# Performance work log

Measured on AMD Instinct MI355X. Metric: run time of the kernel, lower is better.

## Reference

```python
import jax, jax.numpy as jnp
import numpy as np

D = 160          # SDF grid resolution (D1=D2=D3=D)
LEVEL = 0.0      # marching_cubes(-sdf, level=-0) == level 0 on s = -sdf
N_SMOOTH = 2
LAMBD = 1.0


def _extract_mesh_np():
    """Host-side isosurface extraction (mirrors the module's CPU round-trip).
    Uses marching tetrahedra (6-tet cube decomposition) in place of skimage's
    lewiner marching cubes; topo_correct (undefined in source) is identity.
    Returns (verts [V,3] f32 in normalized coords, faces [F,3] i32, edges [E,2] i32).
    """
    xs = np.arange(D, dtype=np.float32)
    X, Y, Z = np.meshgrid(xs, xs, xs, indexing='ij')
    ctr = (D - 1) / 2.0
    sdf = np.sqrt((X - ctr) ** 2 + (Y - ctr) ** 2 + (Z - ctr) ** 2) - 0.35 * D
    sdf = sdf + 3.0 * np.sin(0.20 * X) * np.sin(0.17 * Y) * np.sin(0.23 * Z)
    s = (-sdf).astype(np.float32)  # extract level-0 isosurface of -sdf
    sflat = s.ravel()
    Ng = D ** 3

    corner_off = [(0, 0, 0), (1, 0, 0), (1, 1, 0), (0, 1, 0),
                  (0, 0, 1), (1, 0, 1), (1, 1, 1), (0, 1, 1)]
    b = np.arange(D - 1)
    BX, BY, BZ = np.meshgrid(b, b, b, indexing='ij')
    BX, BY, BZ = BX.ravel(), BY.ravel(), BZ.ravel()
    gid8 = [((BX + dx) * D + (BY + dy)) * D + (BZ + dz) for dx, dy, dz in corner_off]
    val8 = [sflat[g] for g in gid8]

    TETS = [(0, 5, 1, 6), (0, 1, 2, 6), (0, 2, 3, 6),
            (0, 3, 7, 6), (0, 7, 4, 6), (0, 4, 5, 6)]
    TE = [(0, 1), (0, 2), (0, 3), (1, 2), (1, 3), (2, 3)]  # tet edges
    CASE_TRIS = {1: [(0, 1, 2)], 14: [(0, 1, 2)],
                 2: [(0, 3, 4)], 13: [(0, 3, 4)],
                 4: [(1, 3, 5)], 11: [(1, 3, 5)],
                 8: [(2, 4, 5)], 7: [(2, 4, 5)],
                 3: [(1, 3, 4), (1, 4, 2)], 12: [(1, 3, 4), (1, 4, 2)],
                 5: [(0, 3, 5), (0, 5, 2)], 10: [(0, 3, 5), (0, 5, 2)],
                 6: [(0, 4, 5), (0, 5, 1)], 9: [(0, 4, 5), (0, 5, 1)]}
    bitw = np.array([1, 2, 4, 8])

    tri_keys = []
    for tet in TETS:
        tv = np.stack([val8[c] for c in tet], 1)  # [Nc,4] corner values
        tg = np.stack([gid8[c] for c in tet], 1)  # [Nc,4] corner grid ids
        case = (tv < LEVEL).astype(np.int64) @ bitw
        for c, tris in CASE_TRIS.items():
            sel = np.nonzero(case == c)[0]
            if sel.size == 0:
                continue
            g = tg[sel]
            for tri in tris:
                cols = []
                for e in tri:
                    i, j = TE[e]
                    lo = np.minimum(g[:, i], g[:, j])
                    hi = np.maximum(g[:, i], g[:, j])
                    cols.append(lo * Ng + hi)  # canonical grid-edge key
                tri_keys.append(np.stack(cols, 1))
    tris = np.concatenate(tri_keys, 0)  # [F,3] edge keys
    uk, inv = np.unique(tris, return_inverse=True)
    faces = inv.reshape(-1, 3).astype(np.int32)
    ga = uk // Ng
    gb = uk % Ng
    pa = np.stack(np.unravel_index(ga, (D, D, D)), 1).astype(np.float32)
    pb = np.stack(np.unravel_index(gb, (D, D, D)), 1).astype(np.float32)
    sa = sflat[ga]
    sb = sflat[gb]
    t = ((LEVEL - sa) / (sb - sa)).astype(np.float32)
    verts = pa + t[:, None] * (pb - pa)
    verts = (2.0 * verts - np.float32(D)) / np.float32(D)  # (2v-[D1,D2,D3])/D
    e = np.concatenate([faces[:, [0, 1]], faces[:, [1, 2]], faces[:, [2, 0]]], 0)
    e = np.unique(np.sort(e, 1), axis=0).astype(np.int32)
    return verts.astype(np.float32), faces, e


def setup_inputs() -> dict:
    verts, faces, edges = _extract_mesh_np()
    return {
        'v': jnp.asarray(verts)[None],      # [1,V,3]
        'edges': jnp.asarray(edges),        # [E,2] unique undirected mesh edges
        'faces': jnp.asarray(faces)[None],  # [1,F,3]
    }


def reference(v, edges, faces):
    # Uniform laplacian smoothing: v <- v + lambd * (mean_neighbor(v) - v), x2
    V = v.shape[1]
    src = jnp.concatenate([edges[:, 0], edges[:, 1]])
    dst = jnp.concatenate([edges[:, 1], edges[:, 0]])
    x = v[0]
    deg = jax.ops.segment_sum(jnp.ones(src.shape[0], x.dtype), src, num_segments=V)
    inv_deg = 1.0 / jnp.maximum(deg, 1.0)
    for _ in range(N_SMOOTH):
        nbr = jax.ops.segment_sum(x[dst], src, num_segments=V)
        x = x + LAMBD * (nbr * inv_deg[:, None] - x)
    return x, faces[0]
```

## Files before the change

kernel.cpp:

```cpp
#include <hip/hip_runtime.h>
#include <stdint.h>

#define K_ELL 32
#define K_OVF 16
#define RNG   2048
#define RW    (RNG + RNG)
#define BB    256
#define UA    6
#define UN    6
#define UF    4
#define GBS   1024
#define HALO  4096
#define SPAN  (GBS + 2 * HALO)
#define SMEM_STG (SPAN * (int)sizeof(float4))

__global__ __launch_bounds__(BB) void build_kernel(
        const int2* __restrict__ edges, int* __restrict__ offs_a,
        int* __restrict__ cntN, int* __restrict__ cntF, int* __restrict__ deg_ovf,
        int* __restrict__ adjN, int* __restrict__ adjF, int* __restrict__ adj_ovf,
        const int* __restrict__ faces, float* __restrict__ out_f,
        const float* __restrict__ v, float4* __restrict__ v4,
        int E, int V, int F3) {
    const int t = (int)blockIdx.x * BB + (int)threadIdx.x;
    const int T = (int)gridDim.x * BB;
    for (int i = t; i < E; i += T) {
        int2 e = edges[i];
        int rel = e.y - (e.x & ~(RNG - 1)) - 1;
        if (rel < RNG) {
            int r = atomicAdd(&cntN[e.y], 1);
            if (r < K_ELL) adjN[(size_t)r * V + e.y] = e.x;
        } else if (rel < RW) {
            int r = atomicAdd(&cntF[e.y], 1);
            if (r < K_ELL) adjF[(size_t)r * V + e.y] = e.x;
        } else {
            int r = atomicAdd(&deg_ovf[e.y], 1);
            if (r < K_OVF) adj_ovf[(size_t)r * V + e.y] = e.x;
        }
    }
    for (int i = t; i <= E; i += T) {
        if (i < E) {
            int lo = (i == 0) ? 0 : edges[i - 1].x + 1;
            int hi = edges[i].x;
            for (int a = lo; a <= hi; ++a) offs_a[a] = i;
        } else {
            int lo = (E > 0) ? edges[E - 1].x + 1 : 0;
            for (int a = lo; a <= V; ++a) offs_a[a] = E;
        }
    }
    if ((((uintptr_t)out_f | (uintptr_t)faces) & 15) == 0) {
        int n4 = F3 >> 2;
        const int4* f4 = (const int4*)faces;
        float4* o4 = (float4*)out_f;
        for (int j = t; j < n4; j += T) {
            int4 a = f4[j];
            o4[j] = make_float4((float)a.x, (float)a.y, (float)a.z, (float)a.w);
        }
        for (int j = (n4 << 2) + t; j < F3; j += T) out_f[j] = (float)faces[j];
    } else {
        for (int j = t; j < F3; j += T) out_f[j] = (float)faces[j];
    }
    if (((uintptr_t)v & 15) == 0) {
        const float4* vv = (const float4*)v;
        int n4v = V >> 2;
        for (int q = t; q < n4v; q += T) {
            float4 a = vv[3 * q], b = vv[3 * q + 1], c = vv[3 * q + 2];
            v4[4 * q + 0] = make_float4(a.x, a.y, a.z, 0.f);
            v4[4 * q + 1] = make_float4(a.w, b.x, b.y, 0.f);
            v4[4 * q + 2] = make_float4(b.z, b.w, c.x, 0.f);
            v4[4 * q + 3] = make_float4(c.y, c.z, c.w, 0.f);
        }
        for (int u = (n4v << 2) + t; u < V; u += T)
            v4[u] = make_float4(v[3 * u], v[3 * u + 1], v[3 * u + 2], 0.f);
    } else {
        for (int u = t; u < V; u += T)
            v4[u] = make_float4(v[3 * u], v[3 * u + 1], v[3 * u + 2], 0.f);
    }
}

template <bool PAD>
__global__ __launch_bounds__(GBS) void gather_staged(
        const float4* __restrict__ x4, const int2* __restrict__ edges,
        const int* __restrict__ offs_a,
        const int* __restrict__ cntN, const int* __restrict__ cntF,
        const int* __restrict__ deg_ovf,
        const int* __restrict__ adjN, const int* __restrict__ adjF,
        const int* __restrict__ adj_ovf,
        float* __restrict__ y, int V, int E) {
    extern __shared__ float4 tile[];
    const int c0   = (int)blockIdx.x * GBS;
    const int base = c0 - HALO;
    const int u    = c0 + (int)threadIdx.x;
    int aBeg = 0, da = 0, cN = 0, cF = 0, dO = 0;
    int gA[UA], gN[UN], gF[UF];
    if (u < V) {
        aBeg = offs_a[u];
        int aEnd = offs_a[u + 1];
        da = aEnd - aBeg;
        cN = cntN[u]; cF = cntF[u]; dO = deg_ovf[u];
        #pragma unroll
        for (int j = 0; j < UA; ++j) gA[j] = edges[min(aBeg + j, E - 1)].y;
        #pragma unroll
        for (int k = 0; k < UN; ++k) gN[k] = adjN[(size_t)k * V + u];
        #pragma unroll
        for (int k = 0; k < UF; ++k) gF[k] = adjF[(size_t)k * V + u];
    }
    for (int s = (int)threadIdx.x; s < SPAN; s += GBS) {
        int g = base + s;
        tile[s] = (g >= 0 && g < V) ? x4[g] : make_float4(0.f, 0.f, 0.f, 0.f);
    }
    __syncthreads();
    if (u >= V) return;
    int kN = cN > K_ELL ? K_ELL : cN;
    int kF = cF > K_ELL ? K_ELL : cF;
    float s0 = 0.f, s1 = 0.f, s2 = 0.f;
    #pragma unroll
    for (int j = 0; j < UA; ++j) {
        int g = (j < da) ? gA[j] : u;
        float m = (j < da) ? 1.f : 0.f;
        unsigned r = (unsigned)(g - base);
        float4 p = (r < (unsigned)SPAN) ? tile[r] : x4[g];
        s0 += m * p.x; s1 += m * p.y; s2 += m * p.z;
    }
    for (int j = UA; j < da; ++j) {
        float4 p = x4[edges[aBeg + j].y];
        s0 += p.x; s1 += p.y; s2 += p.z;
    }
    #pragma unroll
    for (int k = 0; k < UN; ++k) {
        int g = (k < kN) ? gN[k] : u;
        float m = (k < kN) ? 1.f : 0.f;
        unsigned r = (unsigned)(g - base);
        float4 p = (r < (unsigned)SPAN) ? tile[r] : x4[g];
        s0 += m * p.x; s1 += m * p.y; s2 += m * p.z;
    }
    for (int k = UN; k < kN; ++k) {
        float4 p = x4[adjN[(size_t)k * V + u]];
        s0 += p.x; s1 += p.y; s2 += p.z;
    }
    #pragma unroll
    for (int k = 0; k < UF; ++k) {
        int g = (k < kF) ? gF[k] : u;
        float m = (k < kF) ? 1.f : 0.f;
        unsigned r = (unsigned)(g - base);
        float4 p = (r < (unsigned)SPAN) ? tile[r] : x4[g];
        s0 += m * p.x; s1 += m * p.y; s2 += m * p.z;
    }
    for (int k = UF; k < kF; ++k) {
        float4 p = x4[adjF[(size_t)k * V + u]];
        s0 += p.x; s1 += p.y; s2 += p.z;
    }
    int kO = dO > K_OVF ? K_OVF : dO;
    for (int k = 0; k < kO; ++k) {
        float4 p = x4[adj_ovf[(size_t)k * V + u]];
        s0 += p.x; s1 += p.y; s2 += p.z;
    }
    int d = da + cN + cF + dO;
    float inv = 1.0f / fmaxf((float)d, 1.0f);
    if (PAD) {
        ((float4*)y)[u] = make_float4(s0 * inv, s1 * inv, s2 * inv, 0.f);
    } else {
        y[3 * u + 0] = s0 * inv;
        y[3 * u + 1] = s1 * inv;
        y[3 * u + 2] = s2 * inv;
    }
}

extern "C" void kernel_launch(void* const* d_in, const int* in_sizes, int n_in,
                              void* d_out, int out_size, void* d_ws, size_t ws_size,
                              hipStream_t stream) {
    const float* v     = (const float*)d_in[0];
    const int2*  edges = (const int2*)d_in[1];
    const int*   faces = (const int*)d_in[2];

    const int V3 = in_sizes[0];
    const int V  = V3 / 3;
    const int E  = in_sizes[1] / 2;
    const int F3 = in_sizes[2];

    float* out_v = (float*)d_out;
    float* out_f = (float*)d_out + V3;

    float4* v4      = (float4*)d_ws;
    float4* x1      = v4 + V;
    int*    adjN    = (int*)(x1 + V);
    int*    adjF    = adjN + (size_t)K_ELL * V;
    int*    adj_ovf = adjF + (size_t)K_ELL * V;
    int*    offs_a  = adj_ovf + (size_t)K_OVF * V;
    int*    cntN    = offs_a + (V + 1);
    int*    cntF    = cntN + (V + 1);
    int*    deg_ovf = cntF + (V + 1);

    (void)hipMemsetAsync(cntN, 0, (size_t)(3 * V + 2) * sizeof(int), stream);

    int maxWork = E + 1;
    if (F3 > maxWork) maxWork = F3;
    if (V > maxWork)  maxWork = V;
    int gB = (maxWork + BB - 1) / BB;
    if (gB > 2048) gB = 2048;
    build_kernel<<<gB, BB, 0, stream>>>(edges, offs_a, cntN, cntF, deg_ovf,
                                        adjN, adjF, adj_ovf, faces, out_f,
                                        v, v4, E, V, F3);

    int gS = (V + GBS - 1) / GBS;
    gather_staged<true ><<<gS, GBS, SMEM_STG, stream>>>(
        v4, edges, offs_a, cntN, cntF, deg_ovf, adjN, adjF, adj_ovf,
        (float*)x1, V, E);
    gather_staged<false><<<gS, GBS, SMEM_STG, stream>>>(
        x1, edges, offs_a, cntN, cntF, deg_ovf, adjN, adjF, adj_ovf,
        out_v, V, E);
}
```

Baseline: 104.1 us.

## Merge near/far adjacency lists and drop shared-memory staging in gather

Replaces the three reverse-adjacency ELL tables (near, far, overflow keyed by index distance) with a single ELL table plus an overflow table. The gather kernel no longer stages a halo window of vertex positions in LDS; it reads neighbours straight from global memory through the cache, using 256-thread blocks with no shared memory. This removes the large per-block LDS fill, the barrier and the range-check branching, and it raises occupancy. In exchange, neighbour reads that were LDS hits now go to L2/global, and the memset is smaller.

New measurement: 97.06 us. 1.07x faster.

```diff
diff --git a/kernel.cpp b/kernel.cpp
--- a/kernel.cpp
+++ b/kernel.cpp
@@ -3,21 +3,14 @@
 
 #define K_ELL 32
 #define K_OVF 16
-#define RNG   2048
-#define RW    (RNG + RNG)
 #define BB    256
+#define BS    256
 #define UA    6
-#define UN    6
-#define UF    4
-#define GBS   1024
-#define HALO  4096
-#define SPAN  (GBS + 2 * HALO)
-#define SMEM_STG (SPAN * (int)sizeof(float4))
+#define UB    6
 
 __global__ __launch_bounds__(BB) void build_kernel(
         const int2* __restrict__ edges, int* __restrict__ offs_a,
-        int* __restrict__ cntN, int* __restrict__ cntF, int* __restrict__ deg_ovf,
-        int* __restrict__ adjN, int* __restrict__ adjF, int* __restrict__ adj_ovf,
+        int* __restrict__ cnt, int* __restrict__ adj, int* __restrict__ ovf,
         const int* __restrict__ faces, float* __restrict__ out_f,
         const float* __restrict__ v, float4* __restrict__ v4,
         int E, int V, int F3) {
@@ -25,17 +18,9 @@
     const int T = (int)gridDim.x * BB;
     for (int i = t; i < E; i += T) {
         int2 e = edges[i];
-        int rel = e.y - (e.x & ~(RNG - 1)) - 1;
-        if (rel < RNG) {
-            int r = atomicAdd(&cntN[e.y], 1);
-            if (r < K_ELL) adjN[(size_t)r * V + e.y] = e.x;
-        } else if (rel < RW) {
-            int r = atomicAdd(&cntF[e.y], 1);
-            if (r < K_ELL) adjF[(size_t)r * V + e.y] = e.x;
-        } else {
-            int r = atomicAdd(&deg_ovf[e.y], 1);
-            if (r < K_OVF) adj_ovf[(size_t)r * V + e.y] = e.x;
-        }
+        int r = atomicAdd(&cnt[e.y], 1);
+        if (r < K_ELL)              adj[(size_t)r * V + e.y] = e.x;
+        else if (r < K_ELL + K_OVF) ovf[(size_t)(r - K_ELL) * V + e.y] = e.x;
     }
     for (int i = t; i <= E; i += T) {
         if (i < E) {
@@ -78,47 +63,26 @@
 }
 
 template <bool PAD>
-__global__ __launch_bounds__(GBS) void gather_staged(
-        const float4* __restrict__ x4, const int2* __restrict__ edges,
-        const int* __restrict__ offs_a,
-        const int* __restrict__ cntN, const int* __restrict__ cntF,
-        const int* __restrict__ deg_ovf,
-        const int* __restrict__ adjN, const int* __restrict__ adjF,
-        const int* __restrict__ adj_ovf,
-        float* __restrict__ y, int V, int E) {
-    extern __shared__ float4 tile[];
-    const int c0   = (int)blockIdx.x * GBS;
-    const int base = c0 - HALO;
-    const int u    = c0 + (int)threadIdx.x;
-    int aBeg = 0, da = 0, cN = 0, cF = 0, dO = 0;
-    int gA[UA], gN[UN], gF[UF];
-    if (u < V) {
-        aBeg = offs_a[u];
-        int aEnd = offs_a[u + 1];
-        da = aEnd - aBeg;
-        cN = cntN[u]; cF = cntF[u]; dO = deg_ovf[u];
-        #pragma unroll
-        for (int j = 0; j < UA; ++j) gA[j] = edges[min(aBeg + j, E - 1)].y;
-        #pragma unroll
-        for (int k = 0; k < UN; ++k) gN[k] = adjN[(size_t)k * V + u];
-        #pragma unroll
-        for (int k = 0; k < UF; ++k) gF[k] = adjF[(size_t)k * V + u];
-    }
-    for (int s = (int)threadIdx.x; s < SPAN; s += GBS) {
-        int g = base + s;
-        tile[s] = (g >= 0 && g < V) ? x4[g] : make_float4(0.f, 0.f, 0.f, 0.f);
-    }
-    __syncthreads();
+__global__ void gather_kernel(const float4* __restrict__ x4, const int2* __restrict__ edges,
+                              const int* __restrict__ offs_a, const int* __restrict__ cnt,
+                              const int* __restrict__ adj, const int* __restrict__ ovf,
+                              float* __restrict__ y, int V, int E) {
+    int u = blockIdx.x * blockDim.x + threadIdx.x;
     if (u >= V) return;
-    int kN = cN > K_ELL ? K_ELL : cN;
-    int kF = cF > K_ELL ? K_ELL : cF;
+    int aBeg = offs_a[u], aEnd = offs_a[u + 1];
+    int c = cnt[u];
+    int da = aEnd - aBeg;
+    int kB = c > K_ELL ? K_ELL : c;
+    int gA[UA], gB[UB];
+    #pragma unroll
+    for (int j = 0; j < UA; ++j) gA[j] = edges[min(aBeg + j, E - 1)].y;
+    #pragma unroll
+    for (int k = 0; k < UB; ++k) gB[k] = adj[(size_t)k * V + u];
     float s0 = 0.f, s1 = 0.f, s2 = 0.f;
     #pragma unroll
     for (int j = 0; j < UA; ++j) {
-        int g = (j < da) ? gA[j] : u;
         float m = (j < da) ? 1.f : 0.f;
-        unsigned r = (unsigned)(g - base);
-        float4 p = (r < (unsigned)SPAN) ? tile[r] : x4[g];
+        float4 p = x4[gA[j]];
         s0 += m * p.x; s1 += m * p.y; s2 += m * p.z;
     }
     for (int j = UA; j < da; ++j) {
@@ -126,35 +90,23 @@
         s0 += p.x; s1 += p.y; s2 += p.z;
     }
     #pragma unroll
-    for (int k = 0; k < UN; ++k) {
-        int g = (k < kN) ? gN[k] : u;
-        float m = (k < kN) ? 1.f : 0.f;
-        unsigned r = (unsigned)(g - base);
-        float4 p = (r < (unsigned)SPAN) ? tile[r] : x4[g];
+    for (int k = 0; k < UB; ++k) {
+        float m = (k < kB) ? 1.f : 0.f;
+        float4 p = x4[(k < kB) ? gB[k] : 0];
         s0 += m * p.x; s1 += m * p.y; s2 += m * p.z;
     }
-    for (int k = UN; k < kN; ++k) {
-        float4 p = x4[adjN[(size_t)k * V + u]];
+    for (int k = UB; k < kB; ++k) {
+        float4 p = x4[adj[(size_t)k * V + u]];
         s0 += p.x; s1 += p.y; s2 += p.z;
     }
-    #pragma unroll
-    for (int k = 0; k < UF; ++k) {
-        int g = (k < kF) ? gF[k] : u;
-        float m = (k < kF) ? 1.f : 0.f;
-        unsigned r = (unsigned)(g - base);
-        float4 p = (r < (unsigned)SPAN) ? tile[r] : x4[g];
-        s0 += m * p.x; s1 += m * p.y; s2 += m * p.z;
+    if (c > K_ELL) {
+        int kO = c - K_ELL; if (kO > K_OVF) kO = K_OVF;
+        for (int k = 0; k < kO; ++k) {
+            float4 p = x4[ovf[(size_t)k * V + u]];
+            s0 += p.x; s1 += p.y; s2 += p.z;
+        }
     }
-    for (int k = UF; k < kF; ++k) {
-        float4 p = x4[adjF[(size_t)k * V + u]];
-        s0 += p.x; s1 += p.y; s2 += p.z;
-    }
-    int kO = dO > K_OVF ? K_OVF : dO;
-    for (int k = 0; k < kO; ++k) {
-        float4 p = x4[adj_ovf[(size_t)k * V + u]];
-        s0 += p.x; s1 += p.y; s2 += p.z;
-    }
-    int d = da + cN + cF + dO;
+    int d = da + c;
     float inv = 1.0f / fmaxf((float)d, 1.0f);
     if (PAD) {
         ((float4*)y)[u] = make_float4(s0 * inv, s1 * inv, s2 * inv, 0.f);
@@ -180,32 +132,26 @@
     float* out_v = (float*)d_out;
     float* out_f = (float*)d_out + V3;
 
-    float4* v4      = (float4*)d_ws;
-    float4* x1      = v4 + V;
-    int*    adjN    = (int*)(x1 + V);
-    int*    adjF    = adjN + (size_t)K_ELL * V;
-    int*    adj_ovf = adjF + (size_t)K_ELL * V;
-    int*    offs_a  = adj_ovf + (size_t)K_OVF * V;
-    int*    cntN    = offs_a + (V + 1);
-    int*    cntF    = cntN + (V + 1);
-    int*    deg_ovf = cntF + (V + 1);
+    float4* v4     = (float4*)d_ws;
+    float4* x1     = v4 + V;
+    int*    adj    = (int*)(x1 + V);
+    int*    ovf    = adj + (size_t)K_ELL * V;
+    int*    offs_a = ovf + (size_t)K_OVF * V;
+    int*    cnt    = offs_a + (V + 1);
 
-    (void)hipMemsetAsync(cntN, 0, (size_t)(3 * V + 2) * sizeof(int), stream);
+    (void)hipMemsetAsync(cnt, 0, (size_t)V * sizeof(int), stream);
 
     int maxWork = E + 1;
     if (F3 > maxWork) maxWork = F3;
     if (V > maxWork)  maxWork = V;
     int gB = (maxWork + BB - 1) / BB;
     if (gB > 2048) gB = 2048;
-    build_kernel<<<gB, BB, 0, stream>>>(edges, offs_a, cntN, cntF, deg_ovf,
-                                        adjN, adjF, adj_ovf, faces, out_f,
-                                        v, v4, E, V, F3);
+    build_kernel<<<gB, BB, 0, stream>>>(edges, offs_a, cnt, adj, ovf,
+                                        faces, out_f, v, v4, E, V, F3);
 
-    int gS = (V + GBS - 1) / GBS;
-    gather_staged<true ><<<gS, GBS, SMEM_STG, stream>>>(
-        v4, edges, offs_a, cntN, cntF, deg_ovf, adjN, adjF, adj_ovf,
-        (float*)x1, V, E);
-    gather_staged<false><<<gS, GBS, SMEM_STG, stream>>>(
-        x1, edges, offs_a, cntN, cntF, deg_ovf, adjN, adjF, adj_ovf,
-        out_v, V, E);
+    int gV = (V + BS - 1) / BS;
+    gather_kernel<true ><<<gV, BS, 0, stream>>>(v4, edges, offs_a, cnt, adj, ovf,
+                                                (float*)x1, V, E);
+    gather_kernel<false><<<gV, BS, 0, stream>>>(x1, edges, offs_a, cnt, adj, ovf,
+                                                out_v, V, E);
 }
```
